# Optimization experiments

Hardware: AMD Instinct MI355X
Metric: run time of the kernel (lower is better)

## Reference

```python
import jax, jax.numpy as jnp
import numpy as np

N_NODES = 100000
N_EDGES = 1600000
D_FEAT = 256
UNITS = 128


def setup_inputs() -> dict:
    key = jax.random.key(0)
    k1, k2, k3, k4, k5 = jax.random.split(key, 5)
    x = jax.random.normal(k1, (N_NODES, D_FEAT), dtype=jnp.float32)
    # glorot-scale init for w (scale doesn't affect correctness checking)
    w = jax.random.normal(k2, (D_FEAT, UNITS), dtype=jnp.float32) * (2.0 / (D_FEAT + UNITS)) ** 0.5
    adj_src = jax.random.randint(k3, (N_EDGES,), 0, N_NODES, dtype=jnp.int64)
    adj_dst = jax.random.randint(k4, (N_EDGES,), 0, N_NODES, dtype=jnp.int64)
    adj_vals = jax.random.uniform(k5, (N_EDGES,), dtype=jnp.float32)
    return {"x": x, "w": w, "adj_src": adj_src, "adj_dst": adj_dst, "adj_vals": adj_vals}


def reference(x, w, adj_src, adj_dst, adj_vals):
    # x: [N, D], w: [D, U]  -> dense projection
    h = x @ w  # [N, U]
    # sparse_dense_matmul(adj_norm, h): out[i] = sum_j A[i,j] * h[j]
    # COO: edge e contributes adj_vals[e] * h[adj_src[e]] to row adj_dst[e]
    msgs = adj_vals[:, None] * h[adj_src]  # [E, U]
    out = jax.ops.segment_sum(msgs, adj_dst, num_segments=N_NODES)  # [N, U]
    return out
```

## Files before the change

kernel.cpp:

```cpp
#include <hip/hip_runtime.h>

#define D_FEAT 256
#define UNITS  128

#define NBITS  6
#define BINSZ  64
#define BINCAP 1280
#define MAXNB  1600

typedef __attribute__((ext_vector_type(8))) short short8;
typedef __attribute__((ext_vector_type(4))) float floatx4;

__device__ inline ushort f2bf(float f) {
    uint u = __float_as_uint(f);
    uint r = u + 0x7FFF + ((u >> 16) & 1);
    return (ushort)(r >> 16);
}

__global__ __launch_bounds__(256) void wt_prep_kernel(const float* __restrict__ w,
                                                      ushort* __restrict__ wT,
                                                      int* __restrict__ cursor, int ncur) {
    int idx = blockIdx.x * 256 + threadIdx.x;
    int n = idx >> 8;
    int k = idx & 255;
    wT[n * 256 + k] = f2bf(w[(size_t)k * UNITS + n]);
    if (idx < ncur) cursor[idx] = 0;
}

__global__ __launch_bounds__(256, 2) void gemm_mfma3_kernel(const float* __restrict__ x,
                                                            const ushort* __restrict__ wT,
                                                            ushort* __restrict__ hb, int M) {
    __shared__ ushort lds_w[128 * 256];

    const int tid  = threadIdx.x;
    const int wave = tid >> 6;
    const int lane = tid & 63;
    const int quad = lane >> 4;
    const int m16  = lane & 15;

    const int row  = blockIdx.x * 64 + wave * 16 + m16;
    const int rowc = row < M ? row : M - 1;
    const float* xr = x + (size_t)rowc * D_FEAT;

    short8 wv[16];
    #pragma unroll
    for (int r = 0; r < 16; ++r)
        wv[r] = *(const short8*)(wT + (size_t)(r * 256 + tid) * 8);
    __builtin_amdgcn_sched_barrier(0);

    float4 xv[16];
    #pragma unroll
    for (int s = 0; s < 8; ++s) {
        const float4* p = (const float4*)(xr + s * 32 + quad * 8);
        xv[2 * s]     = p[0];
        xv[2 * s + 1] = p[1];
    }
    __builtin_amdgcn_sched_barrier(0);

    #pragma unroll
    for (int r = 0; r < 16; ++r) {
        int ci = r * 256 + tid;
        int n  = ci >> 5;
        int ts = (ci & 31) ^ (n & 7);
        *(short8*)(lds_w + n * 256 + ts * 8) = wv[r];
    }
    __builtin_amdgcn_sched_barrier(0);

    short8 afrag[8];
    #pragma unroll
    for (int s = 0; s < 8; ++s) {
        float4 lo = xv[2 * s];
        float4 hi = xv[2 * s + 1];
        union { short8 v; ushort u[8]; } af;
        af.u[0] = f2bf(lo.x); af.u[1] = f2bf(lo.y);
        af.u[2] = f2bf(lo.z); af.u[3] = f2bf(lo.w);
        af.u[4] = f2bf(hi.x); af.u[5] = f2bf(hi.y);
        af.u[6] = f2bf(hi.z); af.u[7] = f2bf(hi.w);
        afrag[s] = af.v;
    }

    __syncthreads();

    floatx4 acc[8] = {};
    #pragma unroll
    for (int s = 0; s < 8; ++s) {
        #pragma unroll
        for (int c = 0; c < 8; ++c) {
            int rowb = c * 16 + m16;
            int ts   = (s * 4 + quad) ^ (m16 & 7);
            short8 bfrag = *(const short8*)(lds_w + rowb * 256 + ts * 8);
            acc[c] = __builtin_amdgcn_mfma_f32_16x16x32_bf16(afrag[s], bfrag, acc[c], 0, 0, 0);
        }
    }

    #pragma unroll
    for (int c = 0; c < 8; ++c) {
        #pragma unroll
        for (int i = 0; i < 4; ++i) {
            int r = blockIdx.x * 64 + wave * 16 + quad * 4 + i;
            if (r < M) hb[(size_t)r * UNITS + c * 16 + m16] = f2bf(acc[c][i]);
        }
    }
}

__global__ __launch_bounds__(1024) void coarse_scatter_kernel(const int* __restrict__ src,
                                                              const int* __restrict__ dst,
                                                              const float* __restrict__ vals,
                                                              int* __restrict__ cursor,
                                                              int2* __restrict__ staged,
                                                              int E, int NB, int chunk) {
    __shared__ int s_hist[MAXNB];
    __shared__ int s_base[MAXNB];

    const int tid = threadIdx.x;
    const int T   = 1024;
    const int e0 = blockIdx.x * chunk;
    const int e1 = min(E, e0 + chunk);

    for (int i = tid; i < NB; i += T) s_hist[i] = 0;
    __syncthreads();

    for (int e = e0 + tid; e < e1; e += T)
        atomicAdd(&s_hist[dst[e] >> NBITS], 1);
    __syncthreads();

    for (int b = tid; b < NB; b += T) {
        int c = s_hist[b];
        s_base[b] = (c > 0) ? atomicAdd(&cursor[b * 4], c) : 0;
    }
    __syncthreads();
    for (int i = tid; i < NB; i += T) s_hist[i] = 0;
    __syncthreads();

    for (int e = e0 + tid; e < e1; e += T) {
        int d = dst[e];
        int b = d >> NBITS;
        int r = s_base[b] + atomicAdd(&s_hist[b], 1);
        if (r < BINCAP) {
            int meta = src[e] | ((d & (BINSZ - 1)) << 20);
            staged[(size_t)b * BINCAP + r] = make_int2(meta, __float_as_int(vals[e]));
        }
    }
}

#define ACC8(h, v)                                  \
    a0 += (v) * __uint_as_float((h).x << 16);       \
    a1 += (v) * __uint_as_float((h).x & 0xFFFF0000u); \
    a2 += (v) * __uint_as_float((h).y << 16);       \
    a3 += (v) * __uint_as_float((h).y & 0xFFFF0000u); \
    a4 += (v) * __uint_as_float((h).z << 16);       \
    a5 += (v) * __uint_as_float((h).z & 0xFFFF0000u); \
    a6 += (v) * __uint_as_float((h).w << 16);       \
    a7 += (v) * __uint_as_float((h).w & 0xFFFF0000u);

__global__ __launch_bounds__(512) void gather_sort_kernel(const int* __restrict__ cursor,
                                                          const int2* __restrict__ staged,
                                                          const ushort* __restrict__ hb,
                                                          float* __restrict__ out, int N) {
    __shared__ int2 sraw[BINCAP];
    __shared__ int2 sbuf[BINCAP];
    __shared__ int cnt[BINSZ], ofs[BINSZ], cur[BINSZ];
    __shared__ int gofs[8];

    const int b   = blockIdx.x;
    const int tid = threadIdx.x;

    int n = cursor[b * 4];
    if (n > BINCAP) n = BINCAP;

    for (int i = tid; i < BINSZ; i += 512) cnt[i] = 0;
    __syncthreads();

    const int2* sg = staged + (size_t)b * BINCAP;

    for (int i = tid; i < n; i += 512) {
        int2 e = sg[i];
        sraw[i] = e;
        atomicAdd(&cnt[(e.x >> 20) & (BINSZ - 1)], 1);
    }
    __syncthreads();

    if (tid < 8) {
        int s = 0;
        #pragma unroll
        for (int j = 0; j < 8; ++j) s += cnt[tid * 8 + j];
        gofs[tid] = s;
    }
    __syncthreads();
    if (tid == 0) {
        int run = 0;
        #pragma unroll
        for (int g = 0; g < 8; ++g) { int c = gofs[g]; gofs[g] = run; run += c; }
    }
    __syncthreads();
    if (tid < 8) {
        int run = gofs[tid];
        #pragma unroll
        for (int j = 0; j < 8; ++j) {
            int d = tid * 8 + j;
            int c = cnt[d];
            ofs[d] = run; cur[d] = run; run += c;
        }
    }
    __syncthreads();

    for (int i = tid; i < n; i += 512) {
        int2 e = sraw[i];
        int pos = atomicAdd(&cur[(e.x >> 20) & (BINSZ - 1)], 1);
        sbuf[pos] = e;
    }
    __syncthreads();

    const int ex = (tid >> 6) * 4 + ((tid & 63) >> 4);
    const int m  = tid & 15;

    #pragma unroll
    for (int r = 0; r < 2; ++r) {
        int d  = r * 32 + ex;
        int dg = b * BINSZ + d;
        if (dg >= N) continue;
        int start = ofs[d];
        int c     = cnt[d];

        float a0 = 0.f, a1 = 0.f, a2 = 0.f, a3 = 0.f;
        float a4 = 0.f, a5 = 0.f, a6 = 0.f, a7 = 0.f;
        int j = 0;
        for (; j + 8 <= c; j += 8) {
            int2 e0 = sbuf[start + j];
            int2 e1 = sbuf[start + j + 1];
            int2 e2 = sbuf[start + j + 2];
            int2 e3 = sbuf[start + j + 3];
            int2 e4 = sbuf[start + j + 4];
            int2 e5 = sbuf[start + j + 5];
            int2 e6 = sbuf[start + j + 6];
            int2 e7 = sbuf[start + j + 7];
            __builtin_amdgcn_sched_barrier(0);
            uint4 h0 = *(const uint4*)(hb + (size_t)(e0.x & 0xFFFFF) * UNITS + m * 8);
            uint4 h1 = *(const uint4*)(hb + (size_t)(e1.x & 0xFFFFF) * UNITS + m * 8);
            uint4 h2 = *(const uint4*)(hb + (size_t)(e2.x & 0xFFFFF) * UNITS + m * 8);
            uint4 h3 = *(const uint4*)(hb + (size_t)(e3.x & 0xFFFFF) * UNITS + m * 8);
            uint4 h4 = *(const uint4*)(hb + (size_t)(e4.x & 0xFFFFF) * UNITS + m * 8);
            uint4 h5 = *(const uint4*)(hb + (size_t)(e5.x & 0xFFFFF) * UNITS + m * 8);
            uint4 h6 = *(const uint4*)(hb + (size_t)(e6.x & 0xFFFFF) * UNITS + m * 8);
            uint4 h7 = *(const uint4*)(hb + (size_t)(e7.x & 0xFFFFF) * UNITS + m * 8);
            __builtin_amdgcn_sched_barrier(0);
            float v0 = __int_as_float(e0.y);
            float v1 = __int_as_float(e1.y);
            float v2 = __int_as_float(e2.y);
            float v3 = __int_as_float(e3.y);
            float v4 = __int_as_float(e4.y);
            float v5 = __int_as_float(e5.y);
            float v6 = __int_as_float(e6.y);
            float v7 = __int_as_float(e7.y);
            ACC8(h0, v0)
            ACC8(h1, v1)
            ACC8(h2, v2)
            ACC8(h3, v3)
            ACC8(h4, v4)
            ACC8(h5, v5)
            ACC8(h6, v6)
            ACC8(h7, v7)
        }
        if (j + 4 <= c) {
            int2 e0 = sbuf[start + j];
            int2 e1 = sbuf[start + j + 1];
            int2 e2 = sbuf[start + j + 2];
            int2 e3 = sbuf[start + j + 3];
            __builtin_amdgcn_sched_barrier(0);
            uint4 h0 = *(const uint4*)(hb + (size_t)(e0.x & 0xFFFFF) * UNITS + m * 8);
            uint4 h1 = *(const uint4*)(hb + (size_t)(e1.x & 0xFFFFF) * UNITS + m * 8);
            uint4 h2 = *(const uint4*)(hb + (size_t)(e2.x & 0xFFFFF) * UNITS + m * 8);
            uint4 h3 = *(const uint4*)(hb + (size_t)(e3.x & 0xFFFFF) * UNITS + m * 8);
            __builtin_amdgcn_sched_barrier(0);
            float v0 = __int_as_float(e0.y);
            float v1 = __int_as_float(e1.y);
            float v2 = __int_as_float(e2.y);
            float v3 = __int_as_float(e3.y);
            ACC8(h0, v0)
            ACC8(h1, v1)
            ACC8(h2, v2)
            ACC8(h3, v3)
            j += 4;
        }
        for (; j < c; ++j) {
            int2 e0 = sbuf[start + j];
            uint4 h0 = *(const uint4*)(hb + (size_t)(e0.x & 0xFFFFF) * UNITS + m * 8);
            float v0 = __int_as_float(e0.y);
            ACC8(h0, v0)
        }

        float* op = out + (size_t)dg * UNITS + m * 8;
        *(floatx4*)op       = (floatx4){a0, a1, a2, a3};
        *(floatx4*)(op + 4) = (floatx4){a4, a5, a6, a7};
    }
}

extern "C" void kernel_launch(void* const* d_in, const int* in_sizes, int n_in,
                              void* d_out, int out_size, void* d_ws, size_t ws_size,
                              hipStream_t stream) {
    const float* x        = (const float*)d_in[0];
    const float* w        = (const float*)d_in[1];
    const int*   adj_src  = (const int*)d_in[2];
    const int*   adj_dst  = (const int*)d_in[3];
    const float* adj_vals = (const float*)d_in[4];
    float*       out      = (float*)d_out;

    const int M = in_sizes[0] / D_FEAT;
    const int E = in_sizes[2];
    const int NB = (M + BINSZ - 1) >> NBITS;

    char*   ws  = (char*)d_ws;
    ushort* hb  = (ushort*)ws;
    size_t  off = (size_t)M * UNITS * sizeof(ushort);
    off = (off + 255) & ~(size_t)255;
    ushort* wT  = (ushort*)(ws + off);
    off += (size_t)128 * 256 * sizeof(ushort);
    int*    cursor = (int*)(ws + off);
    off += (size_t)NB * 4 * sizeof(int);
    off = (off + 15) & ~(size_t)15;
    int2*   staged = (int2*)(ws + off);

    wt_prep_kernel<<<128, 256, 0, stream>>>(w, wT, cursor, NB * 4);

    gemm_mfma3_kernel<<<(M + 63) / 64, 256, 0, stream>>>(x, wT, hb, M);

    const int NSCAT = 256;
    const int chunk = (E + NSCAT - 1) / NSCAT;
    coarse_scatter_kernel<<<NSCAT, 1024, 0, stream>>>(adj_src, adj_dst, adj_vals,
                                                      cursor, staged, E, NB, chunk);

    gather_sort_kernel<<<NB, 512, 0, stream>>>(cursor, staged, hb, out, M);
}
```

Measured before the change: 284.8 us.

## Fuse GEMM and edge scatter into one heterogeneous launch to overlap them

Merges the dense bf16 MFMA projection kernel and the coarse edge-binning scatter kernel into a single launch. The first blocks do the scatter and the remaining blocks do the GEMM, so the memory-bound scatter can run alongside the GEMM instead of after it, and one launch is saved. Scatter blocks now run with 256 threads instead of 1024. They also inherit the GEMM's 64KB shared memory footprint and launch bounds, which may reduce how many of them run at once.

```diff
diff --git a/kernel.cpp b/kernel.cpp
--- a/kernel.cpp
+++ b/kernel.cpp
@@ -27,18 +27,59 @@
     if (idx < ncur) cursor[idx] = 0;
 }
 
-__global__ __launch_bounds__(256, 2) void gemm_mfma3_kernel(const float* __restrict__ x,
-                                                            const ushort* __restrict__ wT,
-                                                            ushort* __restrict__ hb, int M) {
-    __shared__ ushort lds_w[128 * 256];
-
-    const int tid  = threadIdx.x;
+__global__ __launch_bounds__(256, 2) void gemm_scatter_kernel(
+        const float* __restrict__ x, const ushort* __restrict__ wT,
+        ushort* __restrict__ hb, int M,
+        const int* __restrict__ src, const int* __restrict__ dst,
+        const float* __restrict__ vals,
+        int* __restrict__ cursor, int2* __restrict__ staged,
+        int E, int NB, int chunk, int nscat) {
+    __shared__ __align__(16) char smem[65536];
+    const int tid = threadIdx.x;
+
+    if ((int)blockIdx.x < nscat) {
+        int* s_hist = (int*)smem;
+        int* s_base = s_hist + MAXNB;
+        const int T  = 256;
+        const int e0 = blockIdx.x * chunk;
+        const int e1 = min(E, e0 + chunk);
+
+        for (int i = tid; i < NB; i += T) s_hist[i] = 0;
+        __syncthreads();
+
+        for (int e = e0 + tid; e < e1; e += T)
+            atomicAdd(&s_hist[dst[e] >> NBITS], 1);
+        __syncthreads();
+
+        for (int b = tid; b < NB; b += T) {
+            int c = s_hist[b];
+            s_base[b] = (c > 0) ? atomicAdd(&cursor[b * 4], c) : 0;
+        }
+        __syncthreads();
+        for (int i = tid; i < NB; i += T) s_hist[i] = 0;
+        __syncthreads();
+
+        for (int e = e0 + tid; e < e1; e += T) {
+            int d = dst[e];
+            int b = d >> NBITS;
+            int r = s_base[b] + atomicAdd(&s_hist[b], 1);
+            if (r < BINCAP) {
+                int meta = src[e] | ((d & (BINSZ - 1)) << 20);
+                staged[(size_t)b * BINCAP + r] = make_int2(meta, __float_as_int(vals[e]));
+            }
+        }
+        return;
+    }
+
+    ushort* lds_w = (ushort*)smem;
+
+    const int bid  = blockIdx.x - nscat;
     const int wave = tid >> 6;
     const int lane = tid & 63;
     const int quad = lane >> 4;
     const int m16  = lane & 15;
 
-    const int row  = blockIdx.x * 64 + wave * 16 + m16;
+    const int row  = bid * 64 + wave * 16 + m16;
     const int rowc = row < M ? row : M - 1;
     const float* xr = x + (size_t)rowc * D_FEAT;
 
@@ -97,48 +138,8 @@
     for (int c = 0; c < 8; ++c) {
         #pragma unroll
         for (int i = 0; i < 4; ++i) {
-            int r = blockIdx.x * 64 + wave * 16 + quad * 4 + i;
+            int r = bid * 64 + wave * 16 + quad * 4 + i;
             if (r < M) hb[(size_t)r * UNITS + c * 16 + m16] = f2bf(acc[c][i]);
-        }
-    }
-}
-
-__global__ __launch_bounds__(1024) void coarse_scatter_kernel(const int* __restrict__ src,
-                                                              const int* __restrict__ dst,
-                                                              const float* __restrict__ vals,
-                                                              int* __restrict__ cursor,
-                                                              int2* __restrict__ staged,
-                                                              int E, int NB, int chunk) {
-    __shared__ int s_hist[MAXNB];
-    __shared__ int s_base[MAXNB];
-
-    const int tid = threadIdx.x;
-    const int T   = 1024;
-    const int e0 = blockIdx.x * chunk;
-    const int e1 = min(E, e0 + chunk);
-
-    for (int i = tid; i < NB; i += T) s_hist[i] = 0;
-    __syncthreads();
-
-    for (int e = e0 + tid; e < e1; e += T)
-        atomicAdd(&s_hist[dst[e] >> NBITS], 1);
-    __syncthreads();
-
-    for (int b = tid; b < NB; b += T) {
-        int c = s_hist[b];
-        s_base[b] = (c > 0) ? atomicAdd(&cursor[b * 4], c) : 0;
-    }
-    __syncthreads();
-    for (int i = tid; i < NB; i += T) s_hist[i] = 0;
-    __syncthreads();
-
-    for (int e = e0 + tid; e < e1; e += T) {
-        int d = dst[e];
-        int b = d >> NBITS;
-        int r = s_base[b] + atomicAdd(&s_hist[b], 1);
-        if (r < BINCAP) {
-            int meta = src[e] | ((d & (BINSZ - 1)) << 20);
-            staged[(size_t)b * BINCAP + r] = make_int2(meta, __float_as_int(vals[e]));
         }
     }
 }
@@ -322,12 +323,11 @@
 
     wt_prep_kernel<<<128, 256, 0, stream>>>(w, wT, cursor, NB * 4);
 
-    gemm_mfma3_kernel<<<(M + 63) / 64, 256, 0, stream>>>(x, wT, hb, M);
-
     const int NSCAT = 256;
     const int chunk = (E + NSCAT - 1) / NSCAT;
-    coarse_scatter_kernel<<<NSCAT, 1024, 0, stream>>>(adj_src, adj_dst, adj_vals,
-                                                      cursor, staged, E, NB, chunk);
+    const int NGEMM = (M + 63) / 64;
+    gemm_scatter_kernel<<<NSCAT + NGEMM, 256, 0, stream>>>(
+        x, wT, hb, M, adj_src, adj_dst, adj_vals, cursor, staged, E, NB, chunk, NSCAT);
 
     gather_sort_kernel<<<NB, 512, 0, stream>>>(cursor, staged, hb, out, M);
 }
```

Result: no change. 283.8 us (-0.3%).
